# Kernel tuning notes

Measured on AMD Instinct MI355X. Metric: run time of the kernel, lower is better.

## Reference

```python
import jax, jax.numpy as jnp
import numpy as np

M = 12          # persons per frame
K = 2           # partition channels from conv1da (1024 = 2*512)
D = 512         # GCN channel dim / LSTM hidden
C_IN = 4096     # backbone feature dim
NUM_CLASSES = 8


def setup_inputs() -> dict:
    key = jax.random.key(0)
    ks = jax.random.split(key, 8)
    N, T = 16, 32
    NT = N * T
    base_out = jax.random.normal(ks[0], (NT, M, C_IN), dtype=jnp.float32)
    dist = jax.random.uniform(ks[1], (N, T, 3, K, M, M), dtype=jnp.float32)
    # conv1da: Conv1d(4096 -> 1024, k=1, bias=False) == matmul with [1024, 4096]
    w_a = jax.random.normal(ks[2], (K * D, C_IN), dtype=jnp.float32) * 0.02
    # LSTM(512, 512, 1): torch gate order i, f, g, o
    s = 1.0 / np.sqrt(D)
    w_ih = jax.random.uniform(ks[3], (4 * D, D), minval=-s, maxval=s, dtype=jnp.float32)
    w_hh = jax.random.uniform(ks[4], (4 * D, D), minval=-s, maxval=s, dtype=jnp.float32)
    b_ih = jax.random.uniform(ks[5], (4 * D,), minval=-s, maxval=s, dtype=jnp.float32)
    b_hh = jax.random.uniform(ks[6], (4 * D,), minval=-s, maxval=s, dtype=jnp.float32)
    # gclassifier: Linear(512 -> num_classes)
    w_cls = jax.random.normal(ks[7], (NUM_CLASSES, D), dtype=jnp.float32) * 0.01
    b_cls = jnp.zeros((NUM_CLASSES,), dtype=jnp.float32)
    return {"base_out": base_out, "dist": dist, "w_a": w_a,
            "w_ih": w_ih, "w_hh": w_hh, "b_ih": b_ih, "b_hh": b_hh,
            "w_cls": w_cls, "b_cls": b_cls, "n_videos": N}


def reference(base_out, dist, w_a, w_ih, w_hh, b_ih, b_hh, w_cls, b_cls, n_videos):
    NT = base_out.shape[0]
    N = n_videos
    T = NT // N
    # conv1da (1x1 conv, no bias): [NT, M, 4096] -> [NT, K*D, M] -> [NT, K, D, M]
    node1 = jnp.einsum('nmc,oc->nom', base_out, w_a).reshape(NT, K, D, M)
    # fused three-way adjacency aggregation: node1a + node1b + node1c
    A = (dist[:, :, 2] + dist[:, :, 1] + dist[:, :, 0]).reshape(NT, K, M, M)
    node = jnp.einsum('nkcv,nkvw->ncw', node1, A)  # [NT, D, M]
    node = jax.nn.relu(node)
    # AdaptiveAvgPool1d(1) over the M persons
    pooled = node.mean(axis=2)                      # [NT, D]
    seq = pooled.reshape(N, T, D)
    # torch nn.LSTM default batch_first=False: iterates over axis 0 (N), batch=T
    def step(carry, x_t):
        h, c = carry
        g = x_t @ w_ih.T + b_ih + h @ w_hh.T + b_hh  # [T, 4D]
        i, f, gg, o = jnp.split(g, 4, axis=-1)
        c = jax.nn.sigmoid(f) * c + jax.nn.sigmoid(i) * jnp.tanh(gg)
        h = jax.nn.sigmoid(o) * jnp.tanh(c)
        return (h, c), h
    h0 = jnp.zeros((T, D), dtype=seq.dtype)
    c0 = jnp.zeros((T, D), dtype=seq.dtype)
    _, hs = jax.lax.scan(step, (h0, c0), seq)       # [N, T, D]
    last = hs[:, -1, :]                              # video_feat[:, -1, :]
    return last @ w_cls.T + b_cls                    # [N, num_classes]
```

## Files before the change

### kernel.cpp

```cpp
#include <hip/hip_runtime.h>
#include <math.h>

#define MM 12
#define KK 2
#define DD 512
#define CIN 4096
#define NCLS 8
#define NV 16
#define TT 32

typedef unsigned long long u64;
typedef __attribute__((ext_vector_type(8))) __bf16 bf16x8;
typedef __attribute__((ext_vector_type(4))) float f32x4;

#define PART_F   0
#define POOLED_F 786432
#define TAGA_F   794624
#define TAGB_F   798720
#define TAGD_F   802816
#define HGLOB_F  804864
#define PART_KS_STRIDE (192 * 1024)

#define MFMA_BF16(A, B, C) __builtin_amdgcn_mfma_f32_16x16x32_bf16((A), (B), (C), 0, 0, 0)
#define LOADR(p)      __hip_atomic_load((p), __ATOMIC_RELAXED, __HIP_MEMORY_SCOPE_AGENT)
#define LOADACQ(p)    __hip_atomic_load((p), __ATOMIC_ACQUIRE, __HIP_MEMORY_SCOPE_AGENT)
#define STORER(p, v)  __hip_atomic_store((p), (v), __ATOMIC_RELAXED, __HIP_MEMORY_SCOPE_AGENT)
#define STOREREL(p, v) __hip_atomic_store((p), (v), __ATOMIC_RELEASE, __HIP_MEMORY_SCOPE_AGENT)

__global__ __launch_bounds__(256, 1) void k_fused(
    const float* __restrict__ base_out, const float* __restrict__ dist,
    const float* __restrict__ w_a, const float* __restrict__ w_ih,
    const float* __restrict__ w_hh, const float* __restrict__ b_ih,
    const float* __restrict__ b_hh, const float* __restrict__ w_cls,
    const float* __restrict__ b_cls,
    float* __restrict__ part, float* __restrict__ pooled,
    unsigned* __restrict__ tagA, unsigned* __restrict__ tagB,
    unsigned* __restrict__ tagD, u64* __restrict__ hg64,
    float* __restrict__ out)
{
  const int wg = blockIdx.x;
  const int tid = threadIdx.x;

  __shared__ __align__(16) unsigned short Ah[16 * 40], Al[16 * 40];
  __shared__ __align__(16) unsigned short Bh[192 * 40], Bl[192 * 40];
  __shared__ __align__(16) float whh_s[16][516];
  __shared__ __align__(16) float wih_s[16][516];
  __shared__ __align__(16) float pooled_s[16][520];
  __shared__ float gx_s[16][20];
  __shared__ __align__(16) float h_s[DD];
  __shared__ float dot_s[16];
  __shared__ float Asum_s[KK * MM * MM];

  {
    const int ks = wg >> 6, ot = wg & 63;
    const int cc0 = ks * 1024;
    const int wave = tid >> 6, lane = tid & 63;
    const int jf0 = wave * 3;

    const int sq = tid & 7;
    const int sr = tid >> 3;
    unsigned boff[6];
#pragma unroll
    for (int rep = 0; rep < 6; ++rep) {
      const int j = sr + 32 * rep;
      const int n = j / 12, m = j - n * 12;
      boff[rep] = (unsigned)(((n * TT + 31) * MM + m) * CIN + cc0 + sq * 4);
    }
    const bool aact = tid < 128;
    unsigned aoff = aact ? (unsigned)((ot * 16 + (tid >> 3)) * CIN + cc0 + sq * 4) : 0u;

    f32x4 acc0 = {0.f, 0.f, 0.f, 0.f}, acc1 = acc0, acc2 = acc0;

    float4 pa, pb[6];
    if (aact) pa = *(const float4*)&w_a[aoff];
#pragma unroll
    for (int rep = 0; rep < 6; ++rep) pb[rep] = *(const float4*)&base_out[boff[rep]];

    for (int st = 0; st < 32; ++st) {
      __syncthreads();
      if (aact) {
        const int idx = (tid >> 3) * 40 + sq * 4;
        unsigned ux = __float_as_uint(pa.x), uy = __float_as_uint(pa.y);
        unsigned uz = __float_as_uint(pa.z), uw = __float_as_uint(pa.w);
        *(uint2*)&Ah[idx] = make_uint2((ux >> 16) | (uy & 0xFFFF0000u),
                                       (uz >> 16) | (uw & 0xFFFF0000u));
        unsigned lx = __float_as_uint(pa.x - __uint_as_float(ux & 0xFFFF0000u));
        unsigned ly = __float_as_uint(pa.y - __uint_as_float(uy & 0xFFFF0000u));
        unsigned lz = __float_as_uint(pa.z - __uint_as_float(uz & 0xFFFF0000u));
        unsigned lw = __float_as_uint(pa.w - __uint_as_float(uw & 0xFFFF0000u));
        *(uint2*)&Al[idx] = make_uint2((lx >> 16) | (ly & 0xFFFF0000u),
                                       (lz >> 16) | (lw & 0xFFFF0000u));
      }
#pragma unroll
      for (int rep = 0; rep < 6; ++rep) {
        const int idx = (sr + 32 * rep) * 40 + sq * 4;
        unsigned ux = __float_as_uint(pb[rep].x), uy = __float_as_uint(pb[rep].y);
        unsigned uz = __float_as_uint(pb[rep].z), uw = __float_as_uint(pb[rep].w);
        *(uint2*)&Bh[idx] = make_uint2((ux >> 16) | (uy & 0xFFFF0000u),
                                       (uz >> 16) | (uw & 0xFFFF0000u));
        unsigned lx = __float_as_uint(pb[rep].x - __uint_as_float(ux & 0xFFFF0000u));
        unsigned ly = __float_as_uint(pb[rep].y - __uint_as_float(uy & 0xFFFF0000u));
        unsigned lz = __float_as_uint(pb[rep].z - __uint_as_float(uz & 0xFFFF0000u));
        unsigned lw = __float_as_uint(pb[rep].w - __uint_as_float(uw & 0xFFFF0000u));
        *(uint2*)&Bl[idx] = make_uint2((lx >> 16) | (ly & 0xFFFF0000u),
                                       (lz >> 16) | (lw & 0xFFFF0000u));
      }
      __syncthreads();
      if (st < 31) {
        aoff += 32;
        if (aact) pa = *(const float4*)&w_a[aoff];
#pragma unroll
        for (int rep = 0; rep < 6; ++rep) {
          boff[rep] += 32;
          pb[rep] = *(const float4*)&base_out[boff[rep]];
        }
      }
      const int koff = (lane >> 4) * 8;
      const int fra = (lane & 15) * 40 + koff;
      bf16x8 oh = *(const bf16x8*)&Ah[fra];
      bf16x8 ol = *(const bf16x8*)&Al[fra];
      {
        const int r0 = ((jf0 + 0) * 16 + (lane & 15)) * 40 + koff;
        bf16x8 jh = *(const bf16x8*)&Bh[r0], jl = *(const bf16x8*)&Bl[r0];
        acc0 = MFMA_BF16(jh, oh, acc0);
        acc0 = MFMA_BF16(jh, ol, acc0);
        acc0 = MFMA_BF16(jl, oh, acc0);
      }
      {
        const int r1 = ((jf0 + 1) * 16 + (lane & 15)) * 40 + koff;
        bf16x8 jh = *(const bf16x8*)&Bh[r1], jl = *(const bf16x8*)&Bl[r1];
        acc1 = MFMA_BF16(jh, oh, acc1);
        acc1 = MFMA_BF16(jh, ol, acc1);
        acc1 = MFMA_BF16(jl, oh, acc1);
      }
      {
        const int r2 = ((jf0 + 2) * 16 + (lane & 15)) * 40 + koff;
        bf16x8 jh = *(const bf16x8*)&Bh[r2], jl = *(const bf16x8*)&Bl[r2];
        acc2 = MFMA_BF16(jh, oh, acc2);
        acc2 = MFMA_BF16(jh, ol, acc2);
        acc2 = MFMA_BF16(jl, oh, acc2);
      }
    }
    const int o = ot * 16 + (lane & 15);
    const int jr = (lane >> 4) * 4;
#pragma unroll
    for (int r = 0; r < 4; ++r) {
      part[((size_t)ks * 192 + (jf0 + 0) * 16 + jr + r) * 1024 + o] = acc0[r];
      part[((size_t)ks * 192 + (jf0 + 1) * 16 + jr + r) * 1024 + o] = acc1[r];
      part[((size_t)ks * 192 + (jf0 + 2) * 16 + jr + r) * 1024 + o] = acc2[r];
    }
    __syncthreads();
    if (tid == 0) STOREREL(&tagA[wg * 16], 1u);
  }

  if (wg < 128) {
    for (int f = tid; f < 16 * DD; f += 256) {
      const int rl = f >> 9, col = f & 511;
      const int row = (rl >> 2) * DD + wg * 4 + (rl & 3);
      whh_s[rl][col] = w_hh[(size_t)row * DD + col];
      wih_s[rl][col] = w_ih[(size_t)row * DD + col];
    }
  }

  if (tid < 64) {
    bool done;
    do {
      unsigned a0 = LOADR(&tagA[(tid      ) * 16]);
      unsigned a1 = LOADR(&tagA[(tid +  64) * 16]);
      unsigned a2 = LOADR(&tagA[(tid + 128) * 16]);
      unsigned a3 = LOADR(&tagA[(tid + 192) * 16]);
      done = __all(a0 == 1u && a1 == 1u && a2 == 1u && a3 == 1u);
    } while (!done);
  }
  __syncthreads();
  (void)LOADACQ(&tagA[0]);

  {
    const int n = wg >> 4, cb = (wg & 15) * 32;
    const unsigned dbase = (unsigned)((n * TT + 31) * (3 * KK * MM * MM));
    for (int f = tid; f < KK * MM * MM; f += 256)
      Asum_s[f] = dist[dbase + f] + dist[dbase + KK * MM * MM + f]
                + dist[dbase + 2 * KK * MM * MM + f];
    __syncthreads();
    if (tid < 32) {
      const int c = cb + tid;
      float nd[KK][MM];
#pragma unroll
      for (int k = 0; k < KK; ++k)
#pragma unroll
        for (int v = 0; v < MM; ++v) {
          const size_t off = (size_t)(n * MM + v) * 1024 + k * DD + c;
          nd[k][v] = part[off] + part[off + PART_KS_STRIDE]
                   + part[off + 2 * PART_KS_STRIDE] + part[off + 3 * PART_KS_STRIDE];
        }
      float accm = 0.f;
#pragma unroll
      for (int w = 0; w < MM; ++w) {
        float sw = 0.f;
#pragma unroll
        for (int k = 0; k < KK; ++k)
#pragma unroll
          for (int v = 0; v < MM; ++v) sw += nd[k][v] * Asum_s[(k * MM + v) * MM + w];
        accm += fmaxf(sw, 0.f);
      }
      pooled[n * DD + c] = accm * (1.f / 12.f);
    }
    __syncthreads();
    if (tid == 0) STOREREL(&tagB[wg * 16], 1u);
  }
  if (wg >= 128) return;

  if (tid < 64) {
    bool done;
    do {
      unsigned a0 = LOADR(&tagB[(tid      ) * 16]);
      unsigned a1 = LOADR(&tagB[(tid +  64) * 16]);
      unsigned a2 = LOADR(&tagB[(tid + 128) * 16]);
      unsigned a3 = LOADR(&tagB[(tid + 192) * 16]);
      done = __all(a0 == 1u && a1 == 1u && a2 == 1u && a3 == 1u);
    } while (!done);
  }
  __syncthreads();
  (void)LOADACQ(&tagB[0]);

  for (int f = tid; f < NV * DD; f += 256) pooled_s[f >> 9][f & 511] = pooled[f];
  __syncthreads();
  {
    const int rl = tid & 15, n = tid >> 4;
    const float4* wr = (const float4*)&wih_s[rl][0];
    const float4* pv = (const float4*)&pooled_s[n][0];
    float a = 0.f;
#pragma unroll 8
    for (int q = 0; q < DD / 4; ++q) {
      float4 x = wr[q], y = pv[q];
      a += x.x * y.x + x.y * y.y + x.z * y.z + x.w * y.w;
    }
    const int row = (rl >> 2) * DD + wg * 4 + (rl & 3);
    gx_s[n][rl] = a + b_ih[row] + b_hh[row];
  }
  __syncthreads();

  {
    float c_reg = 0.f;
    const int r = tid >> 4;
    const int lj = tid & 15;

    for (int s = 0; s < NV; ++s) {
      if (s == 0) {
        h_s[tid] = 0.f; h_s[tid + 256] = 0.f;
      } else {
        if (tid < 64) {
          bool done;
          do {
            int t0 = (int)LOADR(&tagD[(tid     ) * 16]);
            int t1 = (int)LOADR(&tagD[(tid + 64) * 16]);
            done = __all(t0 >= s && t1 >= s);
          } while (!done);
        }
        __syncthreads();
        const size_t hb = (size_t)(s - 1) * 512 + 2 * tid;
        u64 v0 = LOADR(&hg64[hb]);
        u64 v1 = LOADR(&hg64[hb + 1]);
        while ((unsigned)v0 != (unsigned)s) v0 = LOADR(&hg64[hb]);
        while ((unsigned)v1 != (unsigned)s) v1 = LOADR(&hg64[hb + 1]);
        *(float2*)&h_s[2 * tid] = make_float2(__uint_as_float((unsigned)(v0 >> 32)),
                                              __uint_as_float((unsigned)(v1 >> 32)));
      }
      __syncthreads();

      float p = 0.f;
      const float4* wrow = (const float4*)&whh_s[r][0];
      const float4* hv4 = (const float4*)h_s;
#pragma unroll
      for (int q = 0; q < 8; ++q) {
        float4 wv = wrow[lj + 16 * q];
        float4 hv = hv4[lj + 16 * q];
        p += wv.x * hv.x + wv.y * hv.y + wv.z * hv.z + wv.w * hv.w;
      }
#pragma unroll
      for (int off = 8; off; off >>= 1) p += __shfl_down(p, off, 16);
      if (lj == 0) dot_s[r] = p;
      __syncthreads();

      if (tid < 4) {
        const float pi = gx_s[s][tid]      + dot_s[tid];
        const float pf = gx_s[s][4 + tid]  + dot_s[4 + tid];
        const float pg = gx_s[s][8 + tid]  + dot_s[8 + tid];
        const float po = gx_s[s][12 + tid] + dot_s[12 + tid];
        const float si = 1.f / (1.f + expf(-pi));
        const float sf = 1.f / (1.f + expf(-pf));
        const float so = 1.f / (1.f + expf(-po));
        c_reg = sf * c_reg + si * tanhf(pg);
        const float hn = so * tanhf(c_reg);
        const u64 pk = ((u64)__float_as_uint(hn) << 32) | (u64)(unsigned)(s + 1);
        STORER(&hg64[(size_t)s * 512 + wg * 4 + tid], pk);
      }
      if (tid == 0) STORER(&tagD[wg * 16], (unsigned)(s + 1));
    }
  }

  if (wg == 0) {
    if (tid < 64) {
      bool done;
      do {
        int t0 = (int)LOADR(&tagD[(tid     ) * 16]);
        int t1 = (int)LOADR(&tagD[(tid + 64) * 16]);
        done = __all(t0 >= NV && t1 >= NV);
      } while (!done);
    }
    __syncthreads();
    u64 vv[32];
#pragma unroll
    for (int q = 0; q < 32; ++q) vv[q] = LOADR(&hg64[tid + 256 * q]);
#pragma unroll
    for (int q = 0; q < 32; ++q) {
      const int f = tid + 256 * q;
      u64 v = vv[q];
      while ((unsigned)v != (unsigned)((f >> 9) + 1)) v = LOADR(&hg64[f]);
      pooled_s[f >> 9][f & 511] = __uint_as_float((unsigned)(v >> 32));
    }
    __syncthreads();
    if (tid < NV * NCLS) {
      const int n = tid >> 3, cl = tid & 7;
      const float4* hv = (const float4*)&pooled_s[n][0];
      const float4* wv = (const float4*)(w_cls + (size_t)cl * DD);
      float a = b_cls[cl];
#pragma unroll 8
      for (int q = 0; q < DD / 4; ++q) {
        float4 x = hv[q], y = wv[q];
        a += x.x * y.x + x.y * y.y + x.z * y.z + x.w * y.w;
      }
      out[tid] = a;
    }
  }
}

extern "C" void kernel_launch(void* const* d_in, const int* in_sizes, int n_in,
                              void* d_out, int out_size, void* d_ws, size_t ws_size,
                              hipStream_t stream) {
  const float* base_out = (const float*)d_in[0];
  const float* dist     = (const float*)d_in[1];
  const float* w_a      = (const float*)d_in[2];
  const float* w_ih     = (const float*)d_in[3];
  const float* w_hh     = (const float*)d_in[4];
  const float* b_ih     = (const float*)d_in[5];
  const float* b_hh     = (const float*)d_in[6];
  const float* w_cls    = (const float*)d_in[7];
  const float* b_cls    = (const float*)d_in[8];
  float* out = (float*)d_out;

  float* ws = (float*)d_ws;
  float* part   = ws + PART_F;
  float* pooled = ws + POOLED_F;
  unsigned* tagA = (unsigned*)(ws + TAGA_F);
  unsigned* tagB = (unsigned*)(ws + TAGB_F);
  unsigned* tagD = (unsigned*)(ws + TAGD_F);
  u64* hg64 = (u64*)(ws + HGLOB_F);

  k_fused<<<dim3(256), 256, 0, stream>>>(base_out, dist, w_a, w_ih, w_hh,
                                         b_ih, b_hh, w_cls, b_cls,
                                         part, pooled, tagA, tagB, tagD, hg64, out);
}
```

Before: 274.2 us.

## Split LSTM into separate 32-block kernel with wider workgroups

The fused persistent kernel is split into a GEMM+pooling kernel and a separate LSTM kernel, which replaces the tagB grid-wide spin barrier with a kernel boundary. The LSTM now runs on 32 workgroups of 1024 threads, each owning 16 hidden units, so each step's cross-workgroup flag polling covers 32 tags instead of 128. The aim is cheaper per-step global synchronisation in the serial recurrence, at the cost of an extra launch and a larger per-block w_hh slice in shared memory. The input-gate projection now reads w_ih directly from global memory.

```diff
diff --git a/kernel.cpp b/kernel.cpp
--- a/kernel.cpp
+++ b/kernel.cpp
@@ -16,9 +16,8 @@
 #define PART_F   0
 #define POOLED_F 786432
 #define TAGA_F   794624
-#define TAGB_F   798720
-#define TAGD_F   802816
-#define HGLOB_F  804864
+#define TAGD_F   798720
+#define HGLOB_F  799232
 #define PART_KS_STRIDE (192 * 1024)
 
 #define MFMA_BF16(A, B, C) __builtin_amdgcn_mfma_f32_16x16x32_bf16((A), (B), (C), 0, 0, 0)
@@ -27,28 +26,17 @@
 #define STORER(p, v)  __hip_atomic_store((p), (v), __ATOMIC_RELAXED, __HIP_MEMORY_SCOPE_AGENT)
 #define STOREREL(p, v) __hip_atomic_store((p), (v), __ATOMIC_RELEASE, __HIP_MEMORY_SCOPE_AGENT)
 
-__global__ __launch_bounds__(256, 1) void k_fused(
+__global__ __launch_bounds__(256, 1) void k_gemm_pool(
     const float* __restrict__ base_out, const float* __restrict__ dist,
-    const float* __restrict__ w_a, const float* __restrict__ w_ih,
-    const float* __restrict__ w_hh, const float* __restrict__ b_ih,
-    const float* __restrict__ b_hh, const float* __restrict__ w_cls,
-    const float* __restrict__ b_cls,
+    const float* __restrict__ w_a,
     float* __restrict__ part, float* __restrict__ pooled,
-    unsigned* __restrict__ tagA, unsigned* __restrict__ tagB,
-    unsigned* __restrict__ tagD, u64* __restrict__ hg64,
-    float* __restrict__ out)
+    unsigned* __restrict__ tagA)
 {
   const int wg = blockIdx.x;
   const int tid = threadIdx.x;
 
   __shared__ __align__(16) unsigned short Ah[16 * 40], Al[16 * 40];
   __shared__ __align__(16) unsigned short Bh[192 * 40], Bl[192 * 40];
-  __shared__ __align__(16) float whh_s[16][516];
-  __shared__ __align__(16) float wih_s[16][516];
-  __shared__ __align__(16) float pooled_s[16][520];
-  __shared__ float gx_s[16][20];
-  __shared__ __align__(16) float h_s[DD];
-  __shared__ float dot_s[16];
   __shared__ float Asum_s[KK * MM * MM];
 
   {
@@ -153,15 +141,6 @@
     if (tid == 0) STOREREL(&tagA[wg * 16], 1u);
   }
 
-  if (wg < 128) {
-    for (int f = tid; f < 16 * DD; f += 256) {
-      const int rl = f >> 9, col = f & 511;
-      const int row = (rl >> 2) * DD + wg * 4 + (rl & 3);
-      whh_s[rl][col] = w_hh[(size_t)row * DD + col];
-      wih_s[rl][col] = w_ih[(size_t)row * DD + col];
-    }
-  }
-
   if (tid < 64) {
     bool done;
     do {
@@ -205,38 +184,50 @@
       }
       pooled[n * DD + c] = accm * (1.f / 12.f);
     }
-    __syncthreads();
-    if (tid == 0) STOREREL(&tagB[wg * 16], 1u);
-  }
-  if (wg >= 128) return;
-
-  if (tid < 64) {
-    bool done;
-    do {
-      unsigned a0 = LOADR(&tagB[(tid      ) * 16]);
-      unsigned a1 = LOADR(&tagB[(tid +  64) * 16]);
-      unsigned a2 = LOADR(&tagB[(tid + 128) * 16]);
-      unsigned a3 = LOADR(&tagB[(tid + 192) * 16]);
-      done = __all(a0 == 1u && a1 == 1u && a2 == 1u && a3 == 1u);
-    } while (!done);
-  }
+  }
+}
+
+__global__ __launch_bounds__(1024, 4) void k_lstm(
+    const float* __restrict__ pooled,
+    const float* __restrict__ w_ih, const float* __restrict__ w_hh,
+    const float* __restrict__ b_ih, const float* __restrict__ b_hh,
+    const float* __restrict__ w_cls, const float* __restrict__ b_cls,
+    unsigned* __restrict__ tagD, u64* __restrict__ hg64,
+    float* __restrict__ out)
+{
+  const int wg = blockIdx.x;
+  const int tid = threadIdx.x;
+
+  __shared__ __align__(16) float whh_s[64][516];
+  __shared__ float gx_s[16][64];
+  __shared__ __align__(16) float h_s[DD];
+  __shared__ float dot_s[64];
+
+  float* scratch = &whh_s[0][0];
+
+  for (int f = tid; f < NV * DD; f += 1024)
+    scratch[(f >> 9) * 516 + (f & 511)] = pooled[f];
   __syncthreads();
-  (void)LOADACQ(&tagB[0]);
-
-  for (int f = tid; f < NV * DD; f += 256) pooled_s[f >> 9][f & 511] = pooled[f];
-  __syncthreads();
+
   {
-    const int rl = tid & 15, n = tid >> 4;
-    const float4* wr = (const float4*)&wih_s[rl][0];
-    const float4* pv = (const float4*)&pooled_s[n][0];
+    const int n = tid & 15, r = tid >> 4;
+    const int grow = (r >> 4) * DD + wg * 16 + (r & 15);
+    const float4* wr = (const float4*)&w_ih[(size_t)grow * DD];
+    const float4* pv = (const float4*)&scratch[n * 516];
     float a = 0.f;
 #pragma unroll 8
     for (int q = 0; q < DD / 4; ++q) {
       float4 x = wr[q], y = pv[q];
       a += x.x * y.x + x.y * y.y + x.z * y.z + x.w * y.w;
     }
-    const int row = (rl >> 2) * DD + wg * 4 + (rl & 3);
-    gx_s[n][rl] = a + b_ih[row] + b_hh[row];
+    gx_s[n][r] = a + b_ih[grow] + b_hh[grow];
+  }
+  __syncthreads();
+
+  for (int f = tid; f < 64 * 128; f += 1024) {
+    const int rr = f >> 7, c4 = (f & 127) * 4;
+    const int grow = (rr >> 4) * DD + wg * 16 + (rr & 15);
+    *(float4*)&whh_s[rr][c4] = *(const float4*)&w_hh[(size_t)grow * DD + c4];
   }
   __syncthreads();
 
@@ -247,24 +238,22 @@
 
     for (int s = 0; s < NV; ++s) {
       if (s == 0) {
-        h_s[tid] = 0.f; h_s[tid + 256] = 0.f;
+        if (tid < DD) h_s[tid] = 0.f;
       } else {
         if (tid < 64) {
           bool done;
           do {
-            int t0 = (int)LOADR(&tagD[(tid     ) * 16]);
-            int t1 = (int)LOADR(&tagD[(tid + 64) * 16]);
-            done = __all(t0 >= s && t1 >= s);
+            int t0 = (int)LOADR(&tagD[(tid & 31) * 16]);
+            done = __all(t0 >= s);
           } while (!done);
         }
         __syncthreads();
-        const size_t hb = (size_t)(s - 1) * 512 + 2 * tid;
-        u64 v0 = LOADR(&hg64[hb]);
-        u64 v1 = LOADR(&hg64[hb + 1]);
-        while ((unsigned)v0 != (unsigned)s) v0 = LOADR(&hg64[hb]);
-        while ((unsigned)v1 != (unsigned)s) v1 = LOADR(&hg64[hb + 1]);
-        *(float2*)&h_s[2 * tid] = make_float2(__uint_as_float((unsigned)(v0 >> 32)),
-                                              __uint_as_float((unsigned)(v1 >> 32)));
+        if (tid < DD) {
+          u64 v = LOADR(&hg64[(size_t)(s - 1) * DD + tid]);
+          while ((unsigned)v != (unsigned)s)
+            v = LOADR(&hg64[(size_t)(s - 1) * DD + tid]);
+          h_s[tid] = __uint_as_float((unsigned)(v >> 32));
+        }
       }
       __syncthreads();
 
@@ -282,18 +271,18 @@
       if (lj == 0) dot_s[r] = p;
       __syncthreads();
 
-      if (tid < 4) {
+      if (tid < 16) {
         const float pi = gx_s[s][tid]      + dot_s[tid];
-        const float pf = gx_s[s][4 + tid]  + dot_s[4 + tid];
-        const float pg = gx_s[s][8 + tid]  + dot_s[8 + tid];
-        const float po = gx_s[s][12 + tid] + dot_s[12 + tid];
+        const float pf = gx_s[s][16 + tid] + dot_s[16 + tid];
+        const float pg = gx_s[s][32 + tid] + dot_s[32 + tid];
+        const float po = gx_s[s][48 + tid] + dot_s[48 + tid];
         const float si = 1.f / (1.f + expf(-pi));
         const float sf = 1.f / (1.f + expf(-pf));
         const float so = 1.f / (1.f + expf(-po));
         c_reg = sf * c_reg + si * tanhf(pg);
         const float hn = so * tanhf(c_reg);
         const u64 pk = ((u64)__float_as_uint(hn) << 32) | (u64)(unsigned)(s + 1);
-        STORER(&hg64[(size_t)s * 512 + wg * 4 + tid], pk);
+        STORER(&hg64[(size_t)s * DD + wg * 16 + tid], pk);
       }
       if (tid == 0) STORER(&tagD[wg * 16], (unsigned)(s + 1));
     }
@@ -303,26 +292,27 @@
     if (tid < 64) {
       bool done;
       do {
-        int t0 = (int)LOADR(&tagD[(tid     ) * 16]);
-        int t1 = (int)LOADR(&tagD[(tid + 64) * 16]);
-        done = __all(t0 >= NV && t1 >= NV);
+        int t0 = (int)LOADR(&tagD[(tid & 31) * 16]);
+        done = __all(t0 >= NV);
       } while (!done);
     }
     __syncthreads();
-    u64 vv[32];
-#pragma unroll
-    for (int q = 0; q < 32; ++q) vv[q] = LOADR(&hg64[tid + 256 * q]);
-#pragma unroll
-    for (int q = 0; q < 32; ++q) {
-      const int f = tid + 256 * q;
-      u64 v = vv[q];
-      while ((unsigned)v != (unsigned)((f >> 9) + 1)) v = LOADR(&hg64[f]);
-      pooled_s[f >> 9][f & 511] = __uint_as_float((unsigned)(v >> 32));
+    if (tid < DD) {
+      u64 vv[NV];
+#pragma unroll
+      for (int n = 0; n < NV; ++n) vv[n] = LOADR(&hg64[(size_t)n * DD + tid]);
+#pragma unroll
+      for (int n = 0; n < NV; ++n) {
+        u64 v = vv[n];
+        while ((unsigned)v != (unsigned)(n + 1))
+          v = LOADR(&hg64[(size_t)n * DD + tid]);
+        scratch[n * 516 + tid] = __uint_as_float((unsigned)(v >> 32));
+      }
     }
     __syncthreads();
     if (tid < NV * NCLS) {
       const int n = tid >> 3, cl = tid & 7;
-      const float4* hv = (const float4*)&pooled_s[n][0];
+      const float4* hv = (const float4*)&scratch[n * 516];
       const float4* wv = (const float4*)(w_cls + (size_t)cl * DD);
       float a = b_cls[cl];
 #pragma unroll 8
@@ -353,11 +343,10 @@
   float* part   = ws + PART_F;
   float* pooled = ws + POOLED_F;
   unsigned* tagA = (unsigned*)(ws + TAGA_F);
-  unsigned* tagB = (unsigned*)(ws + TAGB_F);
   unsigned* tagD = (unsigned*)(ws + TAGD_F);
   u64* hg64 = (u64*)(ws + HGLOB_F);
 
-  k_fused<<<dim3(256), 256, 0, stream>>>(base_out, dist, w_a, w_ih, w_hh,
-                                         b_ih, b_hh, w_cls, b_cls,
-                                         part, pooled, tagA, tagB, tagD, hg64, out);
+  k_gemm_pool<<<dim3(256), 256, 0, stream>>>(base_out, dist, w_a, part, pooled, tagA);
+  k_lstm<<<dim3(32), 1024, 0, stream>>>(pooled, w_ih, w_hh, b_ih, b_hh,
+                                        w_cls, b_cls, tagD, hg64, out);
 }
```

New measurement: 292.1 us. +6.5%, slower.
